# Optimization experiments

Hardware: AMD Instinct MI355X
Metric: run time of the kernel (lower is better)

The kernel has to match this reference:

```python
import jax, jax.numpy as jnp
import numpy as np

B, T, D, H = 2, 2048, 1024, 16
DH = D // H

def setup_inputs() -> dict:
    key = jax.random.key(0)
    ks = jax.random.split(key, 5)
    s = 1.0 / np.sqrt(D)
    return {
        "x": jax.random.normal(ks[0], (B, T, D), dtype=jnp.float32),
        "w_q": jax.random.normal(ks[1], (D, D), dtype=jnp.float32) * s,
        "w_k": jax.random.normal(ks[2], (D, D), dtype=jnp.float32) * s,
        "w_v": jax.random.normal(ks[3], (D, D), dtype=jnp.float32) * s,
        "w_o": jax.random.normal(ks[4], (D, D), dtype=jnp.float32) * s,
    }

def reference(x, w_q, w_k, w_v, w_o):
    # Linear(bias=False): y = x @ W.T
    q = jnp.einsum('btd,ed->bte', x, w_q).reshape(B, T, H, DH).transpose(0, 2, 1, 3)
    k = jnp.einsum('btd,ed->bte', x, w_k).reshape(B, T, H, DH).transpose(0, 2, 1, 3)
    v = jnp.einsum('btd,ed->bte', x, w_v).reshape(B, T, H, DH).transpose(0, 2, 1, 3)
    scores = jnp.einsum('bhqd,bhkd->bhqk', q, k) / np.sqrt(DH)  # [B,H,T,T]
    causal = jnp.triu(jnp.ones((T, T), dtype=bool), k=1)
    scores = jnp.where(causal[None, None, :, :], -jnp.inf, scores)
    attn = jax.nn.softmax(scores, axis=-1)
    ctx = jnp.einsum('bhqk,bhkd->bhqd', attn, v)
    ctx = ctx.transpose(0, 2, 1, 3).reshape(B, T, D)
    out = jnp.einsum('btd,ed->bte', ctx, w_o)
    return out
```

## Files before the change

kernel.cpp:

```cpp
#include <hip/hip_runtime.h>
#include <hip/hip_bf16.h>

typedef __bf16 bf16_t;
typedef __attribute__((ext_vector_type(8))) __bf16 bf16x8;
typedef __attribute__((ext_vector_type(4))) __bf16 bf16x4;
typedef __attribute__((ext_vector_type(4))) float f32x4;
typedef __attribute__((ext_vector_type(16))) float f32x16;
typedef __attribute__((ext_vector_type(2))) int i32x2;

#define B_ 2
#define T_ 2048
#define D_ 1024
#define H_ 16
#define DH_ 64
#define RS_ 3072

static __device__ __forceinline__ f32x4 mfma16(bf16x8 a, bf16x8 b, f32x4 c) {
  return __builtin_amdgcn_mfma_f32_16x16x32_bf16(a, b, c, 0, 0, 0);
}
static __device__ __forceinline__ f32x16 mfma32(bf16x8 a, bf16x8 b, f32x16 c) {
  return __builtin_amdgcn_mfma_f32_32x32x16_bf16(a, b, c, 0, 0, 0);
}
static __device__ __forceinline__ void gld16(const bf16_t* g, bf16_t* l) {
  __builtin_amdgcn_global_load_lds(
      (const __attribute__((address_space(1))) unsigned int*)g,
      (__attribute__((address_space(3))) unsigned int*)l, 16, 0, 0);
}
static __device__ __forceinline__ unsigned lds_addr(const bf16_t* p) {
  return (unsigned)(uintptr_t)(const __attribute__((address_space(3))) bf16_t*)p;
}
static __device__ __forceinline__ i32x2 tr64(unsigned a) {
  i32x2 d;
  asm volatile("ds_read_b64_tr_b16 %0, %1" : "=v"(d) : "v"(a));
  return d;
}
static __device__ __forceinline__ i32x2 tr64o(unsigned a) {
  i32x2 d;
  asm volatile("ds_read_b64_tr_b16 %0, %1 offset:128" : "=v"(d) : "v"(a));
  return d;
}
static __device__ __forceinline__ unsigned pk2(float lo, float hi2) {
  unsigned short a = __builtin_bit_cast(unsigned short, (bf16_t)lo);
  unsigned short b = __builtin_bit_cast(unsigned short, (bf16_t)hi2);
  return (unsigned)a | ((unsigned)b << 16);
}

#define WAITV4 { asm volatile("s_waitcnt vmcnt(4)" ::: "memory"); __builtin_amdgcn_sched_barrier(0); }
#define WAITV0 { asm volatile("s_waitcnt vmcnt(0)" ::: "memory"); __builtin_amdgcn_sched_barrier(0); }
#define BAR    { __builtin_amdgcn_s_barrier(); __builtin_amdgcn_sched_barrier(0); }
#define WAITL0 { asm volatile("s_waitcnt lgkmcnt(0)" ::: "memory"); __builtin_amdgcn_sched_barrier(0); }

__global__ __launch_bounds__(256) void cvt_x(const float* __restrict__ in,
                                             bf16_t* __restrict__ out, int n4) {
  int i = blockIdx.x * 256 + threadIdx.x;
  if (i >= n4) return;
  float4 f = reinterpret_cast<const float4*>(in)[i];
  bf16x4 o;
  o[0] = (bf16_t)f.x; o[1] = (bf16_t)f.y; o[2] = (bf16_t)f.z; o[3] = (bf16_t)f.w;
  reinterpret_cast<bf16x4*>(out)[i] = o;
}

__global__ __launch_bounds__(256) void cvt_w4(const float* __restrict__ w0,
                                              const float* __restrict__ w1,
                                              const float* __restrict__ w2,
                                              const float* __restrict__ w3,
                                              bf16_t* __restrict__ out, int n4each) {
  const float* in = blockIdx.y == 0 ? w0 : blockIdx.y == 1 ? w1 : blockIdx.y == 2 ? w2 : w3;
  bf16_t* o = out + (size_t)blockIdx.y * (size_t)n4each * 4;
  int i = blockIdx.x * 256 + threadIdx.x;
  if (i >= n4each) return;
  float4 f = reinterpret_cast<const float4*>(in)[i];
  bf16x4 v;
  v[0] = (bf16_t)f.x; v[1] = (bf16_t)f.y; v[2] = (bf16_t)f.z; v[3] = (bf16_t)f.w;
  reinterpret_cast<bf16x4*>(o)[i] = v;
}

template <bool STORE_F32, bool QSCALE>
__global__ __launch_bounds__(256) void gemm_nt(const bf16_t* __restrict__ A,
                                               const bf16_t* __restrict__ Bm,
                                               void* __restrict__ Cv,
                                               int M, int N, int K) {
  __shared__ __align__(16) bf16_t As[3][128 * 32];
  __shared__ __align__(16) bf16_t Bs[3][128 * 32];
  const int tid = threadIdx.x, lane = tid & 63, wave = tid >> 6;
  const int l15 = lane & 15;
  const int brow = blockIdx.y * 128, bcol = blockIdx.x * 128;
  const int row0 = (wave >> 1) * 64, col0 = (wave & 1) * 64;
  const float cscale = (QSCALE && bcol < 1024) ? 0.18033688011112042f : 1.0f;

  f32x4 acc[4][4];
#pragma unroll
  for (int m = 0; m < 4; ++m)
#pragma unroll
    for (int n = 0; n < 4; ++n) acc[m][n] = f32x4{0.f, 0.f, 0.f, 0.f};

  const int nst = K >> 5;
  const int srow = tid >> 2;
  const int sc8 = (tid & 3) * 8;
  auto stage = [&](int bi, int ks) {
    const int k0 = ks * 32;
#pragma unroll
    for (int i = 0; i < 2; ++i)
      gld16(A + (size_t)(brow + 64 * i + srow) * K + k0 + sc8,
            &As[bi][2048 * i + 512 * wave]);
#pragma unroll
    for (int i = 0; i < 2; ++i)
      gld16(Bm + (size_t)(bcol + 64 * i + srow) * K + k0 + sc8,
            &Bs[bi][2048 * i + 512 * wave]);
  };

  stage(0, 0);
  stage(1, 1);

#pragma unroll 1
  for (int ks = 0; ks < nst; ++ks) {
    if (ks + 1 < nst) { WAITV4 } else { WAITV0 }
    BAR;
    if (ks + 2 < nst) stage((ks + 2) % 3, ks + 2);

    const bf16_t* Ab = &As[ks % 3][0];
    const bf16_t* Bb = &Bs[ks % 3][0];
    const int ko = (lane >> 4) * 8;
    bf16x8 af[4], bfr[4];
#pragma unroll
    for (int m = 0; m < 4; ++m)
      af[m] = *(const bf16x8*)&Ab[(row0 + 16 * m + l15) * 32 + ko];
#pragma unroll
    for (int n = 0; n < 4; ++n)
      bfr[n] = *(const bf16x8*)&Bb[(col0 + 16 * n + l15) * 32 + ko];
    WAITL0;
#pragma unroll
    for (int m = 0; m < 4; ++m)
#pragma unroll
      for (int n = 0; n < 4; ++n) acc[m][n] = mfma16(af[m], bfr[n], acc[m][n]);
  }

  const int crow = brow + row0 + (lane >> 4) * 4;
  const int ccol = bcol + col0 + l15;
#pragma unroll
  for (int m = 0; m < 4; ++m)
#pragma unroll
    for (int n = 0; n < 4; ++n)
#pragma unroll
      for (int r = 0; r < 4; ++r) {
        size_t idx = (size_t)(crow + 16 * m + r) * N + (ccol + 16 * n);
        float v = acc[m][n][r] * cscale;
        if (STORE_F32) reinterpret_cast<float*>(Cv)[idx] = v;
        else reinterpret_cast<bf16_t*>(Cv)[idx] = (bf16_t)v;
      }
}

#define CROW(r) ((((r) & 3) + 8 * ((r) >> 2)) + 4 * hi)

__global__ __launch_bounds__(256, 1) void attn_fwd(const bf16_t* __restrict__ qkv,
                                                   bf16_t* __restrict__ ctx) {
  __shared__ __align__(128) bf16_t KV[3][2][64 * 64];
  const int tid = threadIdx.x;
  const int lane = tid & 63;
  const int wv = tid >> 6;
  const int bh = blockIdx.x, p = blockIdx.y;
  const int b = bh >> 4, h = bh & 15;
  const bf16_t* Qg = qkv + (size_t)b * T_ * RS_ + h * DH_;
  const bf16_t* Kg = Qg + 1024;
  const bf16_t* Vg = Qg + 2048;
  bf16_t* Cg = ctx + (size_t)b * T_ * D_ + h * DH_;

  const int hi = lane >> 5;
  const int l31 = lane & 31;
  const int l15 = lane & 15;

  auto stage = [&](int bi, int kt) {
    bf16_t* Kb = &KV[bi][0][0];
    bf16_t* Vb = &KV[bi][1][0];
#pragma unroll
    for (int i = 0; i < 2; ++i) {
      int c2 = i * 256 + tid;
      int r = c2 >> 3, g8 = (c2 & 7) ^ (r & 7);
      gld16(Kg + (size_t)(kt * 64 + r) * RS_ + g8 * 8, Kb + i * 2048 + wv * 512);
    }
#pragma unroll
    for (int i = 0; i < 2; ++i) {
      int c2 = i * 256 + tid;
      int pn = c2 >> 7, k = (c2 >> 1) & 63, half = c2 & 1;
      gld16(Vg + (size_t)(kt * 64 + k) * RS_ + pn * 16 + half * 8, Vb + i * 2048 + wv * 512);
    }
  };

#pragma unroll 1
  for (int phase = 0; phase < 2; ++phase) {
    const int c = phase ? (63 - 4 * p - wv) : (4 * p + wv);
    const int q0 = c * 32;
    const int mynkt = (c >> 1) + 1;
    const int maxnkt = phase ? (32 - 2 * p) : (2 * p + 2);

    BAR;
    stage(0, 0);
    stage(1, 1);

    bf16x8 qf[4];
#pragma unroll
    for (int d = 0; d < 4; ++d)
      qf[d] = *(const bf16x8*)&Qg[(size_t)(q0 + l31) * RS_ + d * 16 + hi * 8];

    f32x16 o[2];
#pragma unroll
    for (int n = 0; n < 2; ++n)
#pragma unroll
      for (int r = 0; r < 16; ++r) o[n][r] = 0.f;
    float mrow = -1e30f, lsum = 0.f;

#pragma unroll 1
    for (int kt = 0; kt < maxnkt; ++kt) {
      if (kt + 1 < maxnkt) { WAITV4 } else { WAITV0 }
      BAR;
      if (kt + 2 < maxnkt) stage((kt + 2) % 3, kt + 2);

      if (kt < mynkt) {
        const bf16_t* Kb = &KV[kt % 3][0][0];
        bf16x8 kf[2][4];
#pragma unroll
        for (int t = 0; t < 2; ++t)
#pragma unroll
          for (int d = 0; d < 4; ++d) {
            int row = 32 * t + l31;
            int col = ((d * 2 + hi) ^ (row & 7)) * 8;
            kf[t][d] = *(const bf16x8*)&Kb[row * 64 + col];
          }
        bf16x8 vf[2][4];
        {
          unsigned vb = lds_addr(&KV[kt % 3][1][0]);
#pragma unroll
          for (int n2 = 0; n2 < 2; ++n2)
#pragma unroll
            for (int ks = 0; ks < 4; ++ks) {
              int pn = 2 * n2 + (l31 >> 4);
              int k0 = ks * 16 + hi * 8;
              unsigned a = vb + pn * 2048 + k0 * 32 + l15 * 8;
              i32x2 lo = tr64(a);
              i32x2 hi4 = tr64o(a);
              union { unsigned u[4]; bf16x8 v; } uu;
              uu.u[0] = (unsigned)lo[0]; uu.u[1] = (unsigned)lo[1];
              uu.u[2] = (unsigned)hi4[0]; uu.u[3] = (unsigned)hi4[1];
              vf[n2][ks] = uu.v;
            }
        }
        WAITL0;

        f32x16 st[2];
#pragma unroll
        for (int t = 0; t < 2; ++t) {
#pragma unroll
          for (int r = 0; r < 16; ++r) st[t][r] = 0.f;
#pragma unroll
          for (int d = 0; d < 4; ++d) st[t] = mfma32(kf[t][d], qf[d], st[t]);
        }
        if (kt == mynkt - 1) {
#pragma unroll
          for (int t = 0; t < 2; ++t)
#pragma unroll
            for (int r = 0; r < 16; ++r)
              if (kt * 64 + 32 * t + CROW(r) > q0 + l31) st[t][r] = -1e30f;
        }
        float pm = -1e30f;
#pragma unroll
        for (int t = 0; t < 2; ++t)
#pragma unroll
          for (int r = 0; r < 16; ++r) pm = fmaxf(pm, st[t][r]);
        pm = fmaxf(pm, __shfl_xor(pm, 32));
        if (!__all(pm - mrow <= 11.0f)) {
          float mn = fmaxf(mrow, pm);
          float scl = exp2f(mrow - mn);
          mrow = mn;
          lsum *= scl;
#pragma unroll
          for (int r = 0; r < 16; ++r) {
            float sr = __shfl(scl, CROW(r));
            o[0][r] *= sr;
            o[1][r] *= sr;
          }
        }
        float ps = 0.f;
#pragma unroll
        for (int t = 0; t < 2; ++t)
#pragma unroll
          for (int r = 0; r < 16; ++r) {
            float e = exp2f(st[t][r] - mrow);
            st[t][r] = e;
            ps += e;
          }
        ps += __shfl_xor(ps, 32);
        lsum += ps;
        unsigned pk[2][8];
#pragma unroll
        for (int t = 0; t < 2; ++t)
#pragma unroll
          for (int j = 0; j < 8; ++j) pk[t][j] = pk2(st[t][2 * j], st[t][2 * j + 1]);
#pragma unroll
        for (int ks = 0; ks < 4; ++ks) {
          const int t = ks >> 1, rb = (ks & 1) * 4;
          unsigned s0 = hi ? pk[t][rb] : pk[t][rb + 2];
          unsigned s1 = hi ? pk[t][rb + 1] : pk[t][rb + 3];
          unsigned r0 = (unsigned)__shfl_xor((int)s0, 32);
          unsigned r1 = (unsigned)__shfl_xor((int)s1, 32);
          union { unsigned u[4]; bf16x8 v; } w;
          if (hi == 0) {
            w.u[0] = pk[t][rb]; w.u[1] = pk[t][rb + 1]; w.u[2] = r0; w.u[3] = r1;
          } else {
            w.u[0] = r0; w.u[1] = r1; w.u[2] = pk[t][rb + 2]; w.u[3] = pk[t][rb + 3];
          }
          o[0] = mfma32(w.v, vf[0][ks], o[0]);
          o[1] = mfma32(w.v, vf[1][ks], o[1]);
        }
      }
    }

#pragma unroll
    for (int r = 0; r < 16; ++r) {
      float li = __shfl(lsum, CROW(r));
      float inv = 1.0f / li;
      int qrow = q0 + CROW(r);
#pragma unroll
      for (int n2 = 0; n2 < 2; ++n2)
        Cg[(size_t)qrow * D_ + n2 * 32 + l31] = (bf16_t)(o[n2][r] * inv);
    }
  }
}

extern "C" void kernel_launch(void* const* d_in, const int* in_sizes, int n_in,
                              void* d_out, int out_size, void* d_ws, size_t ws_size,
                              hipStream_t stream) {
  const float* x   = (const float*)d_in[0];
  const float* w_q = (const float*)d_in[1];
  const float* w_k = (const float*)d_in[2];
  const float* w_v = (const float*)d_in[3];
  const float* w_o = (const float*)d_in[4];

  const int M = B_ * T_;
  const size_t XN = (size_t)M * D_;
  const size_t WN = (size_t)D_ * D_;

  bf16_t* ws = (bf16_t*)d_ws;
  bf16_t* xb   = ws;
  bf16_t* wqb  = xb + XN;
  bf16_t* wob  = wqb + 3 * WN;
  bf16_t* qkv  = wob + WN;
  bf16_t* ctx  = qkv + (size_t)M * RS_;

  cvt_x<<<(int)(XN / 4 / 256), 256, 0, stream>>>(x, xb, (int)(XN / 4));
  cvt_w4<<<dim3((int)(WN / 4 / 256), 4), 256, 0, stream>>>(w_q, w_k, w_v, w_o, wqb, (int)(WN / 4));

  gemm_nt<false, true><<<dim3(RS_ / 128, M / 128), 256, 0, stream>>>(xb, wqb, qkv, M, RS_, D_);

  attn_fwd<<<dim3(B_ * H_, 8), 256, 0, stream>>>(qkv, ctx);

  gemm_nt<true, false><<<dim3(D_ / 128, M / 128), 256, 0, stream>>>(ctx, wob, d_out, M, D_, D_);
}
```

Before: 138.9 us.

## Split attention KV tiles across wave pairs and merge partial softmax in LDS

Each block now handles two 32-row query chunks per phase. Two waves share each chunk and take alternating KV tiles, then merge their partial max, sum and output accumulators through shared memory before normalising. The grid doubles to 16 blocks per head, and launch bounds allow two blocks per CU. This aims for better load balance and occupancy across the causal triangle, at the cost of extra LDS traffic, barriers and merge arithmetic, and half the waves sitting idle on alternate tiles.

```diff
diff --git a/kernel.cpp b/kernel.cpp
--- a/kernel.cpp
+++ b/kernel.cpp
@@ -152,13 +152,16 @@
 
 #define CROW(r) ((((r) & 3) + 8 * ((r) >> 2)) + 4 * hi)
 
-__global__ __launch_bounds__(256, 1) void attn_fwd(const bf16_t* __restrict__ qkv,
+__global__ __launch_bounds__(256, 2) void attn_fwd(const bf16_t* __restrict__ qkv,
                                                    bf16_t* __restrict__ ctx) {
-  __shared__ __align__(128) bf16_t KV[3][2][64 * 64];
+  __shared__ __align__(128) bf16_t KV[3][2][4096];
+  __shared__ float sc_o[2][2][16][64];
+  __shared__ float sc_ml[2][2][32];
   const int tid = threadIdx.x;
   const int lane = tid & 63;
   const int wv = tid >> 6;
-  const int bh = blockIdx.x, p = blockIdx.y;
+  const int ci = wv & 1, ks = wv >> 1;
+  const int bh = blockIdx.x, a = blockIdx.y;
   const int b = bh >> 4, h = bh & 15;
   const bf16_t* Qg = qkv + (size_t)b * T_ * RS_ + h * DH_;
   const bf16_t* Kg = Qg + 1024;
@@ -188,10 +191,10 @@
 
 #pragma unroll 1
   for (int phase = 0; phase < 2; ++phase) {
-    const int c = phase ? (63 - 4 * p - wv) : (4 * p + wv);
+    const int c = phase ? (ci ? 32 + a : 31 - a) : (ci ? 63 - a : a);
     const int q0 = c * 32;
-    const int mynkt = (c >> 1) + 1;
-    const int maxnkt = phase ? (32 - 2 * p) : (2 * p + 2);
+    const int nkt = (c >> 1) + 1;
+    const int maxnkt = phase ? (((32 + a) >> 1) + 1) : (((63 - a) >> 1) + 1);
 
     BAR;
     stage(0, 0);
@@ -215,7 +218,7 @@
       BAR;
       if (kt + 2 < maxnkt) stage((kt + 2) % 3, kt + 2);
 
-      if (kt < mynkt) {
+      if (((kt & 1) == ks) && kt < nkt) {
         const bf16_t* Kb = &KV[kt % 3][0][0];
         bf16x8 kf[2][4];
 #pragma unroll
@@ -232,16 +235,16 @@
 #pragma unroll
           for (int n2 = 0; n2 < 2; ++n2)
 #pragma unroll
-            for (int ks = 0; ks < 4; ++ks) {
+            for (int kss = 0; kss < 4; ++kss) {
               int pn = 2 * n2 + (l31 >> 4);
-              int k0 = ks * 16 + hi * 8;
-              unsigned a = vb + pn * 2048 + k0 * 32 + l15 * 8;
-              i32x2 lo = tr64(a);
-              i32x2 hi4 = tr64o(a);
+              int k0 = kss * 16 + hi * 8;
+              unsigned ad = vb + pn * 2048 + k0 * 32 + l15 * 8;
+              i32x2 lo = tr64(ad);
+              i32x2 hi4 = tr64o(ad);
               union { unsigned u[4]; bf16x8 v; } uu;
               uu.u[0] = (unsigned)lo[0]; uu.u[1] = (unsigned)lo[1];
               uu.u[2] = (unsigned)hi4[0]; uu.u[3] = (unsigned)hi4[1];
-              vf[n2][ks] = uu.v;
+              vf[n2][kss] = uu.v;
             }
         }
         WAITL0;
@@ -254,7 +257,7 @@
 #pragma unroll
           for (int d = 0; d < 4; ++d) st[t] = mfma32(kf[t][d], qf[d], st[t]);
         }
-        if (kt == mynkt - 1) {
+        if (kt == nkt - 1) {
 #pragma unroll
           for (int t = 0; t < 2; ++t)
 #pragma unroll
@@ -296,8 +299,8 @@
 #pragma unroll
           for (int j = 0; j < 8; ++j) pk[t][j] = pk2(st[t][2 * j], st[t][2 * j + 1]);
 #pragma unroll
-        for (int ks = 0; ks < 4; ++ks) {
-          const int t = ks >> 1, rb = (ks & 1) * 4;
+        for (int kss = 0; kss < 4; ++kss) {
+          const int t = kss >> 1, rb = (kss & 1) * 4;
           unsigned s0 = hi ? pk[t][rb] : pk[t][rb + 2];
           unsigned s1 = hi ? pk[t][rb + 1] : pk[t][rb + 3];
           unsigned r0 = (unsigned)__shfl_xor((int)s0, 32);
@@ -308,20 +311,44 @@
           } else {
             w.u[0] = r0; w.u[1] = r1; w.u[2] = pk[t][rb + 2]; w.u[3] = pk[t][rb + 3];
           }
-          o[0] = mfma32(w.v, vf[0][ks], o[0]);
-          o[1] = mfma32(w.v, vf[1][ks], o[1]);
+          o[0] = mfma32(w.v, vf[0][kss], o[0]);
+          o[1] = mfma32(w.v, vf[1][kss], o[1]);
         }
       }
     }
 
-#pragma unroll
-    for (int r = 0; r < 16; ++r) {
-      float li = __shfl(lsum, CROW(r));
-      float inv = 1.0f / li;
-      int qrow = q0 + CROW(r);
+    BAR;
+    if (ks == 1) {
+      if (hi == 0) {
+        sc_ml[ci][0][l31] = mrow;
+        sc_ml[ci][1][l31] = lsum;
+      }
 #pragma unroll
       for (int n2 = 0; n2 < 2; ++n2)
-        Cg[(size_t)qrow * D_ + n2 * 32 + l31] = (bf16_t)(o[n2][r] * inv);
+#pragma unroll
+        for (int r = 0; r < 16; ++r) sc_o[ci][n2][r][lane] = o[n2][r];
+    }
+    BAR;
+    if (ks == 0) {
+      float m1q = sc_ml[ci][0][l31];
+      float l1q = sc_ml[ci][1][l31];
+      float mn = fmaxf(mrow, m1q);
+      float s0 = exp2f(mrow - mn);
+      float s1 = exp2f(m1q - mn);
+      float lf = lsum * s0 + l1q * s1;
+#pragma unroll
+      for (int r = 0; r < 16; ++r) {
+        float s0r = __shfl(s0, CROW(r));
+        float s1r = __shfl(s1, CROW(r));
+        float li = __shfl(lf, CROW(r));
+        float inv = 1.0f / li;
+        int qrow = q0 + CROW(r);
+#pragma unroll
+        for (int n2 = 0; n2 < 2; ++n2) {
+          float of = o[n2][r] * s0r + sc_o[ci][n2][r][lane] * s1r;
+          Cg[(size_t)qrow * D_ + n2 * 32 + l31] = (bf16_t)(of * inv);
+        }
+      }
     }
   }
 }
@@ -351,7 +378,7 @@
 
   gemm_nt<false, true><<<dim3(RS_ / 128, M / 128), 256, 0, stream>>>(xb, wqb, qkv, M, RS_, D_);
 
-  attn_fwd<<<dim3(B_ * H_, 8), 256, 0, stream>>>(qkv, ctx);
+  attn_fwd<<<dim3(B_ * H_, 16), 256, 0, stream>>>(qkv, ctx);
 
   gemm_nt<true, false><<<dim3(D_ / 128, M / 128), 256, 0, stream>>>(ctx, wob, d_out, M, D_, D_);
 }
```

New measurement: 167.2 us. 20.4% more time.

## Merge conversion kernels and deepen GEMM K-tile to 64 with double buffering

Applied to the files above, without the earlier changes.

Replaces the separate x and weight bf16 conversion kernels with one launch covering all eight 1M-element slabs, saving a kernel launch. The GEMM K-step goes from 32 to 64, using two LDS buffers instead of three and issuing 32 MFMAs per barrier instead of 16. This halves the number of barriers and waits per K-loop. The cost is that the loop now waits for all outstanding loads each step (vmcnt 0) with only one stage in flight, so there is less latency hiding, and LDS rows of 64 bf16 may cause more bank conflicts.

```diff
diff --git a/kernel.cpp b/kernel.cpp
--- a/kernel.cpp
+++ b/kernel.cpp
@@ -50,25 +50,17 @@
 #define BAR    { __builtin_amdgcn_s_barrier(); __builtin_amdgcn_sched_barrier(0); }
 #define WAITL0 { asm volatile("s_waitcnt lgkmcnt(0)" ::: "memory"); __builtin_amdgcn_sched_barrier(0); }
 
-__global__ __launch_bounds__(256) void cvt_x(const float* __restrict__ in,
-                                             bf16_t* __restrict__ out, int n4) {
+__global__ __launch_bounds__(256) void cvt_all(const float* __restrict__ x,
+                                               const float* __restrict__ w0,
+                                               const float* __restrict__ w1,
+                                               const float* __restrict__ w2,
+                                               const float* __restrict__ w3,
+                                               bf16_t* __restrict__ out) {
+  const int y = blockIdx.y;
+  const float* in = (y < 4) ? (x + (size_t)y * 1048576)
+                            : (y == 4 ? w0 : y == 5 ? w1 : y == 6 ? w2 : w3);
+  bf16_t* o = out + (size_t)y * 1048576;
   int i = blockIdx.x * 256 + threadIdx.x;
-  if (i >= n4) return;
-  float4 f = reinterpret_cast<const float4*>(in)[i];
-  bf16x4 o;
-  o[0] = (bf16_t)f.x; o[1] = (bf16_t)f.y; o[2] = (bf16_t)f.z; o[3] = (bf16_t)f.w;
-  reinterpret_cast<bf16x4*>(out)[i] = o;
-}
-
-__global__ __launch_bounds__(256) void cvt_w4(const float* __restrict__ w0,
-                                              const float* __restrict__ w1,
-                                              const float* __restrict__ w2,
-                                              const float* __restrict__ w3,
-                                              bf16_t* __restrict__ out, int n4each) {
-  const float* in = blockIdx.y == 0 ? w0 : blockIdx.y == 1 ? w1 : blockIdx.y == 2 ? w2 : w3;
-  bf16_t* o = out + (size_t)blockIdx.y * (size_t)n4each * 4;
-  int i = blockIdx.x * 256 + threadIdx.x;
-  if (i >= n4each) return;
   float4 f = reinterpret_cast<const float4*>(in)[i];
   bf16x4 v;
   v[0] = (bf16_t)f.x; v[1] = (bf16_t)f.y; v[2] = (bf16_t)f.z; v[3] = (bf16_t)f.w;
@@ -80,8 +72,8 @@
                                                const bf16_t* __restrict__ Bm,
                                                void* __restrict__ Cv,
                                                int M, int N, int K) {
-  __shared__ __align__(16) bf16_t As[3][128 * 32];
-  __shared__ __align__(16) bf16_t Bs[3][128 * 32];
+  __shared__ __align__(16) bf16_t As[2][128 * 64];
+  __shared__ __align__(16) bf16_t Bs[2][128 * 64];
   const int tid = threadIdx.x, lane = tid & 63, wave = tid >> 6;
   const int l15 = lane & 15;
   const int brow = blockIdx.y * 128, bcol = blockIdx.x * 128;
@@ -94,45 +86,50 @@
 #pragma unroll
     for (int n = 0; n < 4; ++n) acc[m][n] = f32x4{0.f, 0.f, 0.f, 0.f};
 
-  const int nst = K >> 5;
-  const int srow = tid >> 2;
-  const int sc8 = (tid & 3) * 8;
+  const int nst = K >> 6;
+  const int sr = lane >> 3;
+  const int sc8 = (lane & 7) * 8;
   auto stage = [&](int bi, int ks) {
-    const int k0 = ks * 32;
-#pragma unroll
-    for (int i = 0; i < 2; ++i)
-      gld16(A + (size_t)(brow + 64 * i + srow) * K + k0 + sc8,
-            &As[bi][2048 * i + 512 * wave]);
-#pragma unroll
-    for (int i = 0; i < 2; ++i)
-      gld16(Bm + (size_t)(bcol + 64 * i + srow) * K + k0 + sc8,
-            &Bs[bi][2048 * i + 512 * wave]);
+    const int k0 = ks * 64;
+#pragma unroll
+    for (int i = 0; i < 4; ++i)
+      gld16(A + (size_t)(brow + 32 * i + 8 * wave + sr) * K + k0 + sc8,
+            &As[bi][(32 * i + 8 * wave) * 64]);
+#pragma unroll
+    for (int i = 0; i < 4; ++i)
+      gld16(Bm + (size_t)(bcol + 32 * i + 8 * wave + sr) * K + k0 + sc8,
+            &Bs[bi][(32 * i + 8 * wave) * 64]);
   };
 
   stage(0, 0);
-  stage(1, 1);
 
 #pragma unroll 1
   for (int ks = 0; ks < nst; ++ks) {
-    if (ks + 1 < nst) { WAITV4 } else { WAITV0 }
+    WAITV0;
     BAR;
-    if (ks + 2 < nst) stage((ks + 2) % 3, ks + 2);
-
-    const bf16_t* Ab = &As[ks % 3][0];
-    const bf16_t* Bb = &Bs[ks % 3][0];
-    const int ko = (lane >> 4) * 8;
-    bf16x8 af[4], bfr[4];
-#pragma unroll
-    for (int m = 0; m < 4; ++m)
-      af[m] = *(const bf16x8*)&Ab[(row0 + 16 * m + l15) * 32 + ko];
-#pragma unroll
-    for (int n = 0; n < 4; ++n)
-      bfr[n] = *(const bf16x8*)&Bb[(col0 + 16 * n + l15) * 32 + ko];
+    if (ks + 1 < nst) stage((ks + 1) & 1, ks + 1);
+
+    const bf16_t* Ab = &As[ks & 1][0];
+    const bf16_t* Bb = &Bs[ks & 1][0];
+    bf16x8 af[4][2], bfr[4][2];
+#pragma unroll
+    for (int kk = 0; kk < 2; ++kk) {
+      const int ko = kk * 32 + (lane >> 4) * 8;
+#pragma unroll
+      for (int m = 0; m < 4; ++m)
+        af[m][kk] = *(const bf16x8*)&Ab[(row0 + 16 * m + l15) * 64 + ko];
+#pragma unroll
+      for (int n = 0; n < 4; ++n)
+        bfr[n][kk] = *(const bf16x8*)&Bb[(col0 + 16 * n + l15) * 64 + ko];
+    }
     WAITL0;
 #pragma unroll
-    for (int m = 0; m < 4; ++m)
-#pragma unroll
-      for (int n = 0; n < 4; ++n) acc[m][n] = mfma16(af[m], bfr[n], acc[m][n]);
+    for (int kk = 0; kk < 2; ++kk)
+#pragma unroll
+      for (int m = 0; m < 4; ++m)
+#pragma unroll
+        for (int n = 0; n < 4; ++n)
+          acc[m][n] = mfma16(af[m][kk], bfr[n][kk], acc[m][n]);
   }
 
   const int crow = brow + row0 + (lane >> 4) * 4;
@@ -346,8 +343,7 @@
   bf16_t* qkv  = wob + WN;
   bf16_t* ctx  = qkv + (size_t)M * RS_;
 
-  cvt_x<<<(int)(XN / 4 / 256), 256, 0, stream>>>(x, xb, (int)(XN / 4));
-  cvt_w4<<<dim3((int)(WN / 4 / 256), 4), 256, 0, stream>>>(w_q, w_k, w_v, w_o, wqb, (int)(WN / 4));
+  cvt_all<<<dim3(1024, 8), 256, 0, stream>>>(x, w_q, w_k, w_v, w_o, ws);
 
   gemm_nt<false, true><<<dim3(RS_ / 128, M / 128), 256, 0, stream>>>(xb, wqb, qkv, M, RS_, D_);
 
```

Measured after the change: 153.8 us. 1.11x slower.
